# Performance work log

Hardware: AMD Instinct MI355X
Metric: run time of the kernel (lower is better)

Reference implementation:

```python
import jax, jax.numpy as jnp
import numpy as np

N = 8192
D = 512
H = 256
K_TOPK = 21  # k + 1 with k = 20
EPS_NORM = 1e-12
EPS_DEG = 1e-10


def setup_inputs() -> dict:
    key = jax.random.key(0)
    ks = jax.random.split(key, 10)
    s = 0.02  # small init scale so similarities are well-behaved
    return {
        "features": jax.random.normal(ks[0], (N, D), jnp.float32),
        "masked_features": jax.random.normal(ks[1], (N, D), jnp.float32),
        "W1": jax.random.normal(ks[2], (D, D), jnp.float32) * s,
        "b1": jax.random.normal(ks[3], (D,), jnp.float32) * s,
        "W2": jax.random.normal(ks[4], (D, D), jnp.float32) * s,
        "b2": jax.random.normal(ks[5], (D,), jnp.float32) * s,
        "Wg1": jax.random.normal(ks[6], (D, H), jnp.float32) * s,
        "bg1": jax.random.normal(ks[7], (H,), jnp.float32) * s,
        "Wg2": jax.random.normal(ks[8], (H, D), jnp.float32) * s,
        "bg2": jax.random.normal(ks[9], (D,), jnp.float32) * s,
    }


def reference(features, masked_features, W1, b1, W2, b2, Wg1, bg1, Wg2, bg2):
    # ---- graph generator MLP ----
    h = jax.nn.relu(features @ W1 + b1)            # [N, D]
    emb = h @ W2 + b2                              # [N, D]
    norm = jnp.linalg.norm(emb, axis=1, keepdims=True)
    emb = emb / jnp.maximum(norm, EPS_NORM)        # F.normalize(dim=1, p=2)
    sim = emb @ emb.T                              # [N, N] cosine similarity

    # ---- top-k mask (k+1 neighbors), zero diagonal ----
    _, idx = jax.lax.top_k(sim, K_TOPK)            # [N, K]
    rows = jnp.arange(N)[:, None]
    mask = jnp.zeros((N, N), sim.dtype).at[rows, idx].set(1.0)
    mask = mask * (1.0 - jnp.eye(N, dtype=sim.dtype))  # fill_diagonal_(0)
    mask = jax.lax.stop_gradient(mask)
    sim = jax.nn.relu(sim * mask)

    # ---- symmetrize ----
    gen_adj = (sim + sim.T) * 0.5                  # [N, N]

    # ---- degree norm: D^{-1/2} (A + I) D^{-1/2} ----
    A = gen_adj + jnp.eye(N, dtype=gen_adj.dtype)
    inv_sqrt_deg = 1.0 / (jnp.sqrt(A.sum(axis=1)) + EPS_DEG)
    A = inv_sqrt_deg[:, None] * A * inv_sqrt_deg[None, :]

    # ---- two dense GCN hops (dropout inert in eval mode) ----
    h1 = jax.nn.relu(A @ (masked_features @ Wg1 + bg1))  # [N, H]
    h3 = A @ (h1 @ Wg2 + bg2)                            # [N, D]
    return h3, gen_adj
```

## Files before the change

kernel.cpp:

```cpp
#include <hip/hip_runtime.h>
#include <cstdint>
#include <cstddef>

#define NN 8192
#define DD 512
#define HH 256
#define KTOP 21
#define CCAP 192
#define CMIN 48
#define ECAP 224
#define NBIN 1024
#define BFLOOR 1

typedef __attribute__((ext_vector_type(8))) __bf16 bf16x8;
typedef __attribute__((ext_vector_type(4))) float f32x4;

__device__ __forceinline__ unsigned short f2bf(float x) {
    unsigned u = __float_as_uint(x);
    u += 0x7fffu + ((u >> 16) & 1u);
    return (unsigned short)(u >> 16);
}
__device__ __forceinline__ float bf2f(unsigned short h) {
    return __uint_as_float(((unsigned)h) << 16);
}
__device__ __forceinline__ unsigned ordkey(float x) {
    unsigned b = __float_as_uint(x);
    return b ^ (((int)b >> 31) | 0x80000000u);
}

#define GLD16(gp, lp) __builtin_amdgcn_global_load_lds( \
    (const __attribute__((address_space(1))) unsigned int*)(gp), \
    (__attribute__((address_space(3))) unsigned int*)(lp), 16, 0, 0)

template<bool TRANSB, int ACT>
__global__ __launch_bounds__(256)
void sgemm128(const float* __restrict__ A, const float* __restrict__ B,
              const float* __restrict__ bias, float* __restrict__ C,
              int M, int N, int K) {
    constexpr int BM = 128, BN = 128, BK = 16;
    __shared__ float As[BK][BM + 4];
    __shared__ float Bs[BK][BN + 4];

    const int tiles_n = N / BN;
    const int by = blockIdx.x / tiles_n;
    const int bx = blockIdx.x % tiles_n;
    const int row0 = by * BM, col0 = bx * BN;
    const int tid = threadIdx.x;
    const int tx = tid & 15, ty = tid >> 4;

    float acc[8][8];
#pragma unroll
    for (int m = 0; m < 8; ++m)
#pragma unroll
        for (int n = 0; n < 8; ++n) acc[m][n] = 0.f;

    for (int k0 = 0; k0 < K; k0 += BK) {
#pragma unroll
        for (int l = 0; l < 2; ++l) {
            int f = tid + l * 256;
            int r = f >> 2, c4 = f & 3;
            float4 v = *reinterpret_cast<const float4*>(
                A + (size_t)(row0 + r) * K + k0 + c4 * 4);
            As[c4 * 4 + 0][r] = v.x;
            As[c4 * 4 + 1][r] = v.y;
            As[c4 * 4 + 2][r] = v.z;
            As[c4 * 4 + 3][r] = v.w;
        }
        if (TRANSB) {
#pragma unroll
            for (int l = 0; l < 2; ++l) {
                int f = tid + l * 256;
                int r = f >> 2, c4 = f & 3;
                float4 v = *reinterpret_cast<const float4*>(
                    B + (size_t)(col0 + r) * K + k0 + c4 * 4);
                Bs[c4 * 4 + 0][r] = v.x;
                Bs[c4 * 4 + 1][r] = v.y;
                Bs[c4 * 4 + 2][r] = v.z;
                Bs[c4 * 4 + 3][r] = v.w;
            }
        } else {
#pragma unroll
            for (int l = 0; l < 2; ++l) {
                int f = tid + l * 256;
                int kr = f >> 5, n4 = f & 31;
                *reinterpret_cast<float4*>(&Bs[kr][n4 * 4]) =
                    *reinterpret_cast<const float4*>(
                        B + (size_t)(k0 + kr) * N + col0 + n4 * 4);
            }
        }
        __syncthreads();

#pragma unroll
        for (int kk = 0; kk < BK; ++kk) {
            float a[8], b[8];
            *(float4*)&a[0] = *(const float4*)&As[kk][ty * 8];
            *(float4*)&a[4] = *(const float4*)&As[kk][ty * 8 + 4];
            *(float4*)&b[0] = *(const float4*)&Bs[kk][tx * 8];
            *(float4*)&b[4] = *(const float4*)&Bs[kk][tx * 8 + 4];
#pragma unroll
            for (int m = 0; m < 8; ++m)
#pragma unroll
                for (int n = 0; n < 8; ++n)
                    acc[m][n] = fmaf(a[m], b[n], acc[m][n]);
        }
        __syncthreads();
    }

    const int crow = row0 + ty * 8;
    const int ccol = col0 + tx * 8;
    float bv[8];
#pragma unroll
    for (int n = 0; n < 8; ++n) bv[n] = bias ? bias[ccol + n] : 0.f;
#pragma unroll
    for (int m = 0; m < 8; ++m) {
        float o[8];
#pragma unroll
        for (int n = 0; n < 8; ++n) {
            float t = acc[m][n] + bv[n];
            if (ACT == 1) t = fmaxf(t, 0.f);
            o[n] = t;
        }
        *reinterpret_cast<float4*>(C + (size_t)(crow + m) * N + ccol)     = *(float4*)&o[0];
        *reinterpret_cast<float4*>(C + (size_t)(crow + m) * N + ccol + 4) = *(float4*)&o[4];
    }
}

__global__ __launch_bounds__(256)
void rownorm_emit_kernel(float* __restrict__ emb, unsigned short* __restrict__ ehi) {
    const int row = blockIdx.x, tid = threadIdx.x;
    float* rp = emb + (size_t)row * DD;
    float v0 = rp[tid], v1 = rp[tid + 256];
    float sum = v0 * v0 + v1 * v1;
#pragma unroll
    for (int off = 32; off > 0; off >>= 1) sum += __shfl_down(sum, off, 64);
    __shared__ float ws[4];
    __shared__ float sc_sh;
    if ((tid & 63) == 0) ws[tid >> 6] = sum;
    __syncthreads();
    if (tid == 0) {
        float n = sqrtf(ws[0] + ws[1] + ws[2] + ws[3]);
        sc_sh = 1.0f / fmaxf(n, 1e-12f);
    }
    __syncthreads();
    float sc = sc_sh;
    v0 *= sc; v1 *= sc;
    rp[tid] = v0;
    rp[tid + 256] = v1;
    ehi[(size_t)row * DD + tid]       = f2bf(v0);
    ehi[(size_t)row * DD + tid + 256] = f2bf(v1);
}

__global__ __launch_bounds__(256)
void split_kernel(const float* __restrict__ e, unsigned short* __restrict__ hi,
                  unsigned short* __restrict__ lo) {
    const int i = (blockIdx.x * 256 + threadIdx.x) * 4;
    float4 v = *reinterpret_cast<const float4*>(e + i);
    ushort4 h, l;
    h.x = f2bf(v.x); l.x = f2bf(v.x - bf2f(h.x));
    h.y = f2bf(v.y); l.y = f2bf(v.y - bf2f(h.y));
    h.z = f2bf(v.z); l.z = f2bf(v.z - bf2f(h.z));
    h.w = f2bf(v.w); l.w = f2bf(v.w - bf2f(h.w));
    *reinterpret_cast<ushort4*>(hi + i) = h;
    *reinterpret_cast<ushort4*>(lo + i) = l;
}

__global__ __launch_bounds__(256)
void wtrans_kernel(const float* __restrict__ W, unsigned short* __restrict__ Thi,
                   unsigned short* __restrict__ Tlo, int K, int N) {
    int t = blockIdx.x * 256 + threadIdx.x;
    if (t >= K * N) return;
    int k = t / N, n = t - k * N;
    float x = W[t];
    unsigned short h = f2bf(x);
    Thi[(size_t)n * K + k] = h;
    Tlo[(size_t)n * K + k] = f2bf(x - bf2f(h));
}

__global__ __launch_bounds__(256)
void simgemm_bf16(const unsigned short* __restrict__ Ehi,
                  unsigned short* __restrict__ Cb) {
    const int bid = blockIdx.x;
    const int swz = (bid & 7) * 512 + (bid >> 3);
    const int by = swz >> 6, bx = swz & 63;

    __shared__ unsigned short SB[8192];
    unsigned short* Ah = SB;
    unsigned short* Bh = SB + 4096;

    const int tid = threadIdx.x, lane = tid & 63, wid = tid >> 6;
    const int wm = wid >> 1, wn = wid & 1;
    const int fr = lane & 15, fq = lane >> 4;
    const int lrow = lane >> 2;
    const int lcol8 = (lane & 3) * 8;

    const size_t arow0 = (size_t)by * 128;
    const size_t brow0 = (size_t)bx * 128;

    f32x4 acc[4][4];
#pragma unroll
    for (int m = 0; m < 4; ++m)
#pragma unroll
        for (int n = 0; n < 4; ++n) acc[m][n] = (f32x4){0.f, 0.f, 0.f, 0.f};

    for (int k0 = 0; k0 < DD; k0 += 32) {
#pragma unroll
        for (int i = 0; i < 2; ++i) {
            const int chunk = wid + i * 4;
            const int grow = chunk * 16 + lrow;
            GLD16(Ehi + (arow0 + grow) * DD + (k0 + lcol8), Ah + chunk * 512);
            GLD16(Ehi + (brow0 + grow) * DD + (k0 + lcol8), Bh + chunk * 512);
        }
        __syncthreads();

        bf16x8 ah[4], bh[4];
#pragma unroll
        for (int mf = 0; mf < 4; ++mf)
            ah[mf] = *(const bf16x8*)&Ah[(wm * 64 + mf * 16 + fr) * 32 + fq * 8];
#pragma unroll
        for (int nf = 0; nf < 4; ++nf)
            bh[nf] = *(const bf16x8*)&Bh[(wn * 64 + nf * 16 + fr) * 32 + fq * 8];
#pragma unroll
        for (int mf = 0; mf < 4; ++mf)
#pragma unroll
            for (int nf = 0; nf < 4; ++nf)
                acc[mf][nf] = __builtin_amdgcn_mfma_f32_16x16x32_bf16(ah[mf], bh[nf], acc[mf][nf], 0, 0, 0);
        __syncthreads();
    }

#pragma unroll
    for (int ph = 0; ph < 2; ++ph) {
        if (wm == ph) {
#pragma unroll
            for (int mf = 0; mf < 4; ++mf)
#pragma unroll
                for (int nf = 0; nf < 4; ++nf)
#pragma unroll
                    for (int r2 = 0; r2 < 4; ++r2)
                        SB[(mf * 16 + fq * 4 + r2) * 128 + wn * 64 + nf * 16 + fr] =
                            f2bf(acc[mf][nf][r2]);
        }
        __syncthreads();
#pragma unroll
        for (int it = 0; it < 4; ++it) {
            int flat = it * 256 + tid;
            int rowL = flat >> 4, cc = flat & 15;
            *reinterpret_cast<uint4*>(
                &Cb[(arow0 + ph * 64 + rowL) * NN + (size_t)bx * 128 + cc * 8]) =
                *reinterpret_cast<const uint4*>(&SB[rowL * 128 + cc * 8]);
        }
        __syncthreads();
    }
}

template<int KDIM>
__global__ __launch_bounds__(256)
void mfma_nt_bias(const unsigned short* __restrict__ Ahi,
                  const unsigned short* __restrict__ Alo,
                  const unsigned short* __restrict__ Bhi,
                  const unsigned short* __restrict__ Blo,
                  const float* __restrict__ bias, float* __restrict__ C, int N) {
    const int tiles_n = N / 128;
    const int by = blockIdx.x / tiles_n, bx = blockIdx.x % tiles_n;

    __shared__ unsigned short Ah[128 * 32];
    __shared__ unsigned short Al[128 * 32];
    __shared__ unsigned short Bh[128 * 32];
    __shared__ unsigned short Bl[128 * 32];

    const int tid = threadIdx.x, lane = tid & 63, wid = tid >> 6;
    const int wm = wid >> 1, wn = wid & 1;
    const int fr = lane & 15, fq = lane >> 4;
    const int lrow = lane >> 2;
    const int lcol8 = (lane & 3) * 8;

    const size_t arow0 = (size_t)by * 128;
    const size_t brow0 = (size_t)bx * 128;

    f32x4 acc[4][4];
#pragma unroll
    for (int m = 0; m < 4; ++m)
#pragma unroll
        for (int n = 0; n < 4; ++n) acc[m][n] = (f32x4){0.f, 0.f, 0.f, 0.f};

    for (int k0 = 0; k0 < KDIM; k0 += 32) {
#pragma unroll
        for (int i = 0; i < 2; ++i) {
            const int chunk = wid + i * 4;
            const int grow = chunk * 16 + lrow;
            GLD16(Ahi + (arow0 + grow) * KDIM + (k0 + lcol8), Ah + chunk * 512);
            GLD16(Alo + (arow0 + grow) * KDIM + (k0 + lcol8), Al + chunk * 512);
            GLD16(Bhi + (brow0 + grow) * KDIM + (k0 + lcol8), Bh + chunk * 512);
            GLD16(Blo + (brow0 + grow) * KDIM + (k0 + lcol8), Bl + chunk * 512);
        }
        __syncthreads();

        bf16x8 ah[4], al[4], bh[4], bl[4];
#pragma unroll
        for (int mf = 0; mf < 4; ++mf) {
            const int r = wm * 64 + mf * 16 + fr;
            ah[mf] = *(const bf16x8*)&Ah[r * 32 + fq * 8];
            al[mf] = *(const bf16x8*)&Al[r * 32 + fq * 8];
        }
#pragma unroll
        for (int nf = 0; nf < 4; ++nf) {
            const int r = wn * 64 + nf * 16 + fr;
            bh[nf] = *(const bf16x8*)&Bh[r * 32 + fq * 8];
            bl[nf] = *(const bf16x8*)&Bl[r * 32 + fq * 8];
        }
#pragma unroll
        for (int mf = 0; mf < 4; ++mf)
#pragma unroll
            for (int nf = 0; nf < 4; ++nf) {
                acc[mf][nf] = __builtin_amdgcn_mfma_f32_16x16x32_bf16(ah[mf], bh[nf], acc[mf][nf], 0, 0, 0);
                acc[mf][nf] = __builtin_amdgcn_mfma_f32_16x16x32_bf16(ah[mf], bl[nf], acc[mf][nf], 0, 0, 0);
                acc[mf][nf] = __builtin_amdgcn_mfma_f32_16x16x32_bf16(al[mf], bh[nf], acc[mf][nf], 0, 0, 0);
            }
        __syncthreads();
    }

#pragma unroll
    for (int mf = 0; mf < 4; ++mf) {
#pragma unroll
        for (int nf = 0; nf < 4; ++nf) {
            const size_t row = arow0 + wm * 64 + mf * 16 + fq * 4;
            const int col = bx * 128 + wn * 64 + nf * 16 + fr;
            const float bv = bias[col];
#pragma unroll
            for (int r2 = 0; r2 < 4; ++r2)
                C[(row + r2) * N + col] = acc[mf][nf][r2] + bv;
        }
    }
}

__global__ __launch_bounds__(256)
void topk_refine_kernel(const unsigned short* __restrict__ simb,
                        const float* __restrict__ emb,
                        int* __restrict__ tidx, float* __restrict__ tval,
                        int* __restrict__ ecnt, int* __restrict__ elj,
                        float* __restrict__ elv) {
    const int row = blockIdx.x;
    const int tid = threadIdx.x;
    const int lane = tid & 63, wave = tid >> 6;

    const uint4* rp = reinterpret_cast<const uint4*>(simb + (size_t)row * NN);
    uint4 q[4];
#pragma unroll
    for (int t = 0; t < 4; ++t) q[t] = rp[t * 256 + tid];
    unsigned pk[16];
#pragma unroll
    for (int t = 0; t < 4; ++t) {
        pk[t * 4 + 0] = q[t].x; pk[t * 4 + 1] = q[t].y;
        pk[t * 4 + 2] = q[t].z; pk[t * 4 + 3] = q[t].w;
    }

    __shared__ int hist[NBIN];
    for (int b = tid; b < NBIN; b += 256) hist[b] = 0;
    __syncthreads();

    short bins[32];
#pragma unroll
    for (int u = 0; u < 16; ++u) {
        float flo = __uint_as_float(pk[u] << 16);
        float fhi = __uint_as_float(pk[u] & 0xFFFF0000u);
        int blo = (int)(flo * (float)NBIN); blo = max(0, min(NBIN - 1, blo));
        int bhi = (int)(fhi * (float)NBIN); bhi = max(0, min(NBIN - 1, bhi));
        bins[u * 2]     = (short)blo;
        bins[u * 2 + 1] = (short)bhi;
        if (blo >= BFLOOR) atomicAdd(&hist[blo], 1);
        if (bhi >= BFLOOR) atomicAdd(&hist[bhi], 1);
    }
    __syncthreads();

    __shared__ int s_bstar;
    if (wave == 0) {
        int cum = 0, found = -1;
        for (int c0 = NBIN - 1; c0 >= 0 && found < 0; c0 -= 64) {
            int b = c0 - lane;
            int cnt = (b >= 0) ? hist[b] : 0;
            int sc = cnt;
#pragma unroll
            for (int off = 1; off < 64; off <<= 1) {
                int o = __shfl_up(sc, off, 64);
                if (lane >= off) sc += o;
            }
            int chunk_total = __shfl(sc, 63, 64);
            bool hit = (cum + sc >= CMIN);
            unsigned long long mh = __ballot(hit);
            if (mh) found = c0 - (__ffsll((long long)mh) - 1);
            else cum += chunk_total;
        }
        if (found < 0) found = 0;
        if (lane == 0) s_bstar = found;
    }
    __syncthreads();
    const int bstar = s_bstar;

    __shared__ int s_cand[CCAP];
    int cnt = 0;
#pragma unroll
    for (int i = 0; i < 32; ++i) cnt += (bins[i] >= bstar) ? 1 : 0;
    int sc = cnt;
#pragma unroll
    for (int off = 1; off < 64; off <<= 1) {
        int o = __shfl_up(sc, off, 64);
        if (lane >= off) sc += o;
    }
    __shared__ int wtot[4];
    if (lane == 63) wtot[wave] = sc;
    __syncthreads();
    int base = sc - cnt;
#pragma unroll
    for (int w = 0; w < 4; ++w)
        if (w < wave) base += wtot[w];
    int total = wtot[0] + wtot[1] + wtot[2] + wtot[3];

    int pos = base;
#pragma unroll
    for (int u = 0; u < 16; ++u) {
#pragma unroll
        for (int h = 0; h < 2; ++h) {
            if (bins[u * 2 + h] >= bstar) {
                if (pos < CCAP)
                    s_cand[pos] = ((u >> 2) * 256 + tid) * 8 + (u & 3) * 2 + h;
                pos++;
            }
        }
    }
    __syncthreads();
    const int ncand = min(total, CCAP);

    __shared__ float sval[CCAP];
    __shared__ int   sidx[CCAP];
    const float* ei = emb + (size_t)row * DD;
    float4 a0 = reinterpret_cast<const float4*>(ei)[lane * 2];
    float4 a1 = reinterpret_cast<const float4*>(ei)[lane * 2 + 1];

    for (int base2 = wave * 2; base2 < ncand; base2 += 8) {
#pragma unroll
        for (int qq = 0; qq < 2; ++qq) {
            int c = base2 + qq;
            if (c >= ncand) break;
            const int j = s_cand[c];
            const float* ej = emb + (size_t)j * DD;
            float4 b0 = reinterpret_cast<const float4*>(ej)[lane * 2];
            float4 b1 = reinterpret_cast<const float4*>(ej)[lane * 2 + 1];
            float s = 0.f;
            s = fmaf(a0.x, b0.x, s); s = fmaf(a0.y, b0.y, s);
            s = fmaf(a0.z, b0.z, s); s = fmaf(a0.w, b0.w, s);
            s = fmaf(a1.x, b1.x, s); s = fmaf(a1.y, b1.y, s);
            s = fmaf(a1.z, b1.z, s); s = fmaf(a1.w, b1.w, s);
#pragma unroll
            for (int off = 32; off > 0; off >>= 1) s += __shfl_xor(s, off, 64);
            if (lane == 0) { sval[c] = s; sidx[c] = j; }
        }
    }
    __syncthreads();

    __shared__ float selv[KTOP];
    __shared__ int   seli[KTOP];
    if (wave == 0) {
        float v[3]; int id[3];
#pragma unroll
        for (int k = 0; k < 3; ++k) {
            int s = lane + 64 * k;
            if (s < ncand) { v[k] = sval[s]; id[k] = sidx[s]; }
            else           { v[k] = -INFINITY; id[k] = 0x7fffffff; }
        }
#pragma unroll 1
        for (int sel = 0; sel < KTOP; ++sel) {
            float bv = v[0]; int bi = id[0];
#pragma unroll
            for (int k = 1; k < 3; ++k)
                if (v[k] > bv || (v[k] == bv && id[k] < bi)) { bv = v[k]; bi = id[k]; }
#pragma unroll
            for (int off = 1; off < 64; off <<= 1) {
                float ov = __shfl_xor(bv, off, 64);
                int   oi = __shfl_xor(bi, off, 64);
                if (ov > bv || (ov == bv && oi < bi)) { bv = ov; bi = oi; }
            }
            if (lane == 0) { selv[sel] = bv; seli[sel] = bi; }
#pragma unroll
            for (int k = 0; k < 3; ++k)
                if (id[k] == bi) { v[k] = -INFINITY; id[k] = 0x7fffffff; }
        }
    }
    __syncthreads();

    if (tid < KTOP) {
        float bv = selv[tid];
        int   bi = seli[tid];
        tval[(size_t)row * KTOP + tid] = bv;
        tidx[(size_t)row * KTOP + tid] = bi;
        if (bi != row && bi >= 0 && bi < NN && bv > 0.f) {
            float v = bv * 0.5f;
            int pi = atomicAdd(ecnt + row, 1);
            if (pi < ECAP) { elj[(size_t)row * ECAP + pi] = bi; elv[(size_t)row * ECAP + pi] = v; }
            int pj = atomicAdd(ecnt + bi, 1);
            if (pj < ECAP) { elj[(size_t)bi * ECAP + pj] = row; elv[(size_t)bi * ECAP + pj] = v; }
        }
    }
}

__global__ __launch_bounds__(256)
void sort_write_kernel(int* __restrict__ ej, float* __restrict__ ev,
                       const int* __restrict__ ecnt,
                       float* __restrict__ adj, float* __restrict__ sdeg) {
    const int row = blockIdx.x, tid = threadIdx.x;
    const int nraw = ecnt[row];

    float4* out4 = reinterpret_cast<float4*>(adj + (size_t)row * NN);
    const float4 z = {0.f, 0.f, 0.f, 0.f};
#pragma unroll
    for (int f = tid; f < NN / 4; f += 256) out4[f] = z;

    if (nraw > ECAP) return;

    const int n = nraw;
    __shared__ int   lj[ECAP];
    __shared__ float lv[ECAP];
    __shared__ unsigned long long skey[ECAP];
    __shared__ int   oj[ECAP];
    __shared__ float ov[ECAP];
    if (tid < n) {
        int  jv = ej[(size_t)row * ECAP + tid];
        float vv = ev[(size_t)row * ECAP + tid];
        lj[tid] = jv; lv[tid] = vv;
        skey[tid] = ((unsigned long long)(unsigned)jv << 32) | (unsigned long long)ordkey(vv);
    }
    __syncthreads();
    if (tid < n) {
        unsigned long long mk = skey[tid];
        int rank = 0;
        for (int u = 0; u < n; ++u) {
            unsigned long long ku = skey[u];
            rank += (ku < mk || (ku == mk && u < tid)) ? 1 : 0;
        }
        oj[rank] = lj[tid];
        ov[rank] = lv[tid];
    }
    __syncthreads();
    if (tid < n) {
        ej[(size_t)row * ECAP + tid] = oj[tid];
        ev[(size_t)row * ECAP + tid] = ov[tid];
    }
    if (tid == 0) {
        float deg = 1.0f;
        for (int e = 0; e < n; ++e) deg += ov[e];
        sdeg[row] = 1.0f / (sqrtf(deg) + 1e-10f);
    }
    __syncthreads();
    if (tid < n) {
        int j = oj[tid];
        if (tid == 0 || oj[tid - 1] != j) {
            float s = ov[tid];
            if (tid + 1 < n && oj[tid + 1] == j) s += ov[tid + 1];
            adj[(size_t)row * NN + j] = s;
        }
    }
}

__global__ __launch_bounds__(256)
void ovf_fix_kernel(const int* __restrict__ tidx, const float* __restrict__ tval,
                    const int* __restrict__ ecnt, float* __restrict__ adj) {
    int t = blockIdx.x * 256 + threadIdx.x;
    if (t >= NN * KTOP) return;
    int i = t / KTOP;
    int j = tidx[t];
    if (j == i || j < 0) return;
    float v = tval[t];
    if (v <= 0.f) return;
    v *= 0.5f;
    if (ecnt[i] > ECAP) atomicAdd(adj + (size_t)i * NN + j, v);
    if (ecnt[j] > ECAP) atomicAdd(adj + (size_t)j * NN + i, v);
}

__global__ __launch_bounds__(256)
void ovf_deg_kernel(const int* __restrict__ ecnt, const float* __restrict__ adj,
                    float* __restrict__ sdeg) {
    const int row = blockIdx.x, tid = threadIdx.x;
    if (ecnt[row] <= ECAP) return;
    const int lane = tid & 63, wave = tid >> 6;
    const float4* rp = reinterpret_cast<const float4*>(adj + (size_t)row * NN);
    float sum = 0.f;
    for (int f = tid; f < NN / 4; f += 256) {
        float4 v = rp[f];
        sum += (v.x + v.y) + (v.z + v.w);
    }
#pragma unroll
    for (int off = 32; off > 0; off >>= 1) sum += __shfl_down(sum, off, 64);
    __shared__ float ws[4];
    if (lane == 0) ws[wave] = sum;
    __syncthreads();
    if (tid == 0)
        sdeg[row] = 1.0f / (sqrtf(1.0f + ws[0] + ws[1] + ws[2] + ws[3]) + 1e-10f);
}

template<int COLS, bool DORELU>
__global__ __launch_bounds__(256)
void spmm_edges(const int* __restrict__ ej, const float* __restrict__ ev,
                const int* __restrict__ ecnt, const float* __restrict__ adj,
                const float* __restrict__ sdeg,
                const float* __restrict__ X, float* __restrict__ Y) {
    constexpr int CPT = COLS / 256;
    const int i = blockIdx.x;
    const int tid = threadIdx.x;
    const int lane = tid & 63, wave = tid >> 6;
    const float si = sdeg[i];
    const int nraw = ecnt[i];

    float acc[CPT];
#pragma unroll
    for (int c = 0; c < CPT; ++c) acc[c] = 0.f;

    if (nraw <= ECAP) {
        __shared__ int   s_j[ECAP];
        __shared__ float s_w[ECAP];
        if (tid < nraw) {
            int j = ej[(size_t)i * ECAP + tid];
            s_j[tid] = j;
            s_w[tid] = ev[(size_t)i * ECAP + tid] * sdeg[j];
        }
        __syncthreads();
#pragma unroll 4
        for (int e = 0; e < nraw; ++e) {
            int j = s_j[e];
            float we = s_w[e];
#pragma unroll
            for (int c = 0; c < CPT; ++c)
                acc[c] += we * X[(size_t)j * COLS + tid + c * 256];
        }
    } else {
        __shared__ int   s_j[256];
        __shared__ float s_w[256];
        __shared__ int   s_cnt[4];
        const float* rowp = adj + (size_t)i * NN;
        for (int j0 = 0; j0 < NN; j0 += 256) {
            float w = rowp[j0 + tid];
            bool nz = (w != 0.f);
            unsigned long long m = __ballot(nz);
            unsigned long long ltmask = (lane == 0) ? 0ull : (~0ull >> (64 - lane));
            int pre = __popcll(m & ltmask);
            if (lane == 0) s_cnt[wave] = __popcll(m);
            __syncthreads();
            int base = 0;
#pragma unroll
            for (int q = 0; q < 4; ++q)
                if (q < wave) base += s_cnt[q];
            int total = s_cnt[0] + s_cnt[1] + s_cnt[2] + s_cnt[3];
            if (nz) {
                int p = base + pre;
                s_j[p] = j0 + tid;
                s_w[p] = w * sdeg[j0 + tid];
            }
            __syncthreads();
            for (int e = 0; e < total; ++e) {
                int j = s_j[e];
                float we = s_w[e];
#pragma unroll
                for (int c = 0; c < CPT; ++c)
                    acc[c] += we * X[(size_t)j * COLS + tid + c * 256];
            }
            __syncthreads();
        }
    }

#pragma unroll
    for (int c = 0; c < CPT; ++c) {
        float val = si * (acc[c] + si * X[(size_t)i * COLS + tid + c * 256]);
        if (DORELU) val = fmaxf(val, 0.f);
        Y[(size_t)i * COLS + tid + c * 256] = val;
    }
}

extern "C" void kernel_launch(void* const* d_in, const int* in_sizes, int n_in,
                              void* d_out, int out_size, void* d_ws, size_t ws_size,
                              hipStream_t stream) {
    const float* features = (const float*)d_in[0];
    const float* masked   = (const float*)d_in[1];
    const float* W1  = (const float*)d_in[2];
    const float* b1  = (const float*)d_in[3];
    const float* W2  = (const float*)d_in[4];
    const float* b2  = (const float*)d_in[5];
    const float* Wg1 = (const float*)d_in[6];
    const float* bg1 = (const float*)d_in[7];
    const float* Wg2 = (const float*)d_in[8];
    const float* bg2 = (const float*)d_in[9];

    float* out_h3  = (float*)d_out;
    float* out_adj = (float*)d_out + (size_t)NN * DD;
    unsigned short* simb = (unsigned short*)out_adj;

    float* Areg = (float*)d_ws;
    float* Breg = Areg + (size_t)NN * DD;
    float* tail = Breg + (size_t)NN * DD;

    float* h    = Areg;
    unsigned short* ehi = (unsigned short*)Areg;
    unsigned short* mhi = (unsigned short*)Areg;
    unsigned short* mlo = mhi + (size_t)NN * DD;
    unsigned short* h1hi = (unsigned short*)Areg;
    unsigned short* h1lo = h1hi + (size_t)NN * HH;

    float* emb = Breg;
    float* x1  = Breg;
    float* h1  = Breg + (size_t)NN * HH;
    float* x2  = Breg;

    float* tval = tail;
    int*   tidx = (int*)(tval + (size_t)NN * KTOP);
    float* sdeg = (float*)(tidx + (size_t)NN * KTOP);
    int*   ecnt = (int*)(sdeg + NN);
    int*   elj  = ecnt + NN;
    float* elv  = (float*)(elj + (size_t)NN * ECAP);
    unsigned short* wt1hi = (unsigned short*)(elv + (size_t)NN * ECAP);
    unsigned short* wt1lo = wt1hi + (size_t)HH * DD;
    unsigned short* wt2hi = wt1lo + (size_t)HH * DD;
    unsigned short* wt2lo = wt2hi + (size_t)DD * HH;

    dim3 blk(256);

    sgemm128<false, 1><<<dim3((NN / 128) * (DD / 128)), blk, 0, stream>>>(
        features, W1, b1, h, NN, DD, DD);
    sgemm128<false, 0><<<dim3((NN / 128) * (DD / 128)), blk, 0, stream>>>(
        h, W2, b2, emb, NN, DD, DD);
    rownorm_emit_kernel<<<dim3(NN), blk, 0, stream>>>(emb, ehi);
    simgemm_bf16<<<dim3(4096), blk, 0, stream>>>(ehi, simb);
    hipMemsetAsync(ecnt, 0, (size_t)NN * sizeof(int), stream);
    topk_refine_kernel<<<dim3(NN), blk, 0, stream>>>(
        simb, emb, tidx, tval, ecnt, elj, elv);
    sort_write_kernel<<<dim3(NN), blk, 0, stream>>>(elj, elv, ecnt, out_adj, sdeg);
    ovf_fix_kernel<<<dim3((NN * KTOP + 255) / 256), blk, 0, stream>>>(
        tidx, tval, ecnt, out_adj);
    ovf_deg_kernel<<<dim3(NN), blk, 0, stream>>>(ecnt, out_adj, sdeg);
    split_kernel<<<dim3(NN * DD / 1024), blk, 0, stream>>>(masked, mhi, mlo);
    wtrans_kernel<<<dim3(DD * HH / 256), blk, 0, stream>>>(Wg1, wt1hi, wt1lo, DD, HH);
    mfma_nt_bias<DD><<<dim3((NN / 128) * (HH / 128)), blk, 0, stream>>>(
        mhi, mlo, wt1hi, wt1lo, bg1, x1, HH);
    spmm_edges<HH, true><<<dim3(NN), blk, 0, stream>>>(
        elj, elv, ecnt, out_adj, sdeg, x1, h1);
    split_kernel<<<dim3(NN * HH / 1024), blk, 0, stream>>>(h1, h1hi, h1lo);
    wtrans_kernel<<<dim3(HH * DD / 256), blk, 0, stream>>>(Wg2, wt2hi, wt2lo, HH, DD);
    mfma_nt_bias<HH><<<dim3((NN / 128) * (DD / 128)), blk, 0, stream>>>(
        h1hi, h1lo, wt2hi, wt2lo, bg2, x2, DD);
    spmm_edges<DD, false><<<dim3(NN), blk, 0, stream>>>(
        elj, elv, ecnt, out_adj, sdeg, x2, out_h3);
}
```

Baseline: 734.7 us.

## Compute only upper-triangular similarity tiles and mirror them via swizzled LDS transpose

The bf16 similarity GEMM now launches only the 2080 upper-triangular 128x128 tiles. Each off-diagonal tile is written twice, once directly and once transposed through an XOR-swizzled LDS buffer, using the symmetry of emb·embᵀ to cut MFMA work roughly in half. The ecnt memset is folded into the row-norm kernel, and the two weight-transpose kernels are merged into one launch. The cost is a scattered transposed store pattern with 16-byte writes across rows, plus a small serial loop that maps each block index to its tile.

```diff
diff --git a/kernel.cpp b/kernel.cpp
--- a/kernel.cpp
+++ b/kernel.cpp
@@ -11,6 +11,7 @@
 #define ECAP 224
 #define NBIN 1024
 #define BFLOOR 1
+#define NTRI 2080
 
 typedef __attribute__((ext_vector_type(8))) __bf16 bf16x8;
 typedef __attribute__((ext_vector_type(4))) float f32x4;
@@ -27,6 +28,7 @@
     unsigned b = __float_as_uint(x);
     return b ^ (((int)b >> 31) | 0x80000000u);
 }
+__device__ __forceinline__ int swzc(int r, int c) { return c ^ ((r & 7) << 4); }
 
 #define GLD16(gp, lp) __builtin_amdgcn_global_load_lds( \
     (const __attribute__((address_space(1))) unsigned int*)(gp), \
@@ -126,7 +128,8 @@
 }
 
 __global__ __launch_bounds__(256)
-void rownorm_emit_kernel(float* __restrict__ emb, unsigned short* __restrict__ ehi) {
+void rownorm_emit_kernel(float* __restrict__ emb, unsigned short* __restrict__ ehi,
+                         int* __restrict__ ecnt) {
     const int row = blockIdx.x, tid = threadIdx.x;
     float* rp = emb + (size_t)row * DD;
     float v0 = rp[tid], v1 = rp[tid + 256];
@@ -140,6 +143,7 @@
     if (tid == 0) {
         float n = sqrtf(ws[0] + ws[1] + ws[2] + ws[3]);
         sc_sh = 1.0f / fmaxf(n, 1e-12f);
+        ecnt[row] = 0;
     }
     __syncthreads();
     float sc = sc_sh;
@@ -165,23 +169,34 @@
 }
 
 __global__ __launch_bounds__(256)
-void wtrans_kernel(const float* __restrict__ W, unsigned short* __restrict__ Thi,
-                   unsigned short* __restrict__ Tlo, int K, int N) {
+void wtrans2_kernel(const float* __restrict__ Wg1, const float* __restrict__ Wg2,
+                    unsigned short* __restrict__ t1h, unsigned short* __restrict__ t1l,
+                    unsigned short* __restrict__ t2h, unsigned short* __restrict__ t2l) {
     int t = blockIdx.x * 256 + threadIdx.x;
-    if (t >= K * N) return;
-    int k = t / N, n = t - k * N;
-    float x = W[t];
-    unsigned short h = f2bf(x);
-    Thi[(size_t)n * K + k] = h;
-    Tlo[(size_t)n * K + k] = f2bf(x - bf2f(h));
-}
-
-__global__ __launch_bounds__(256)
-void simgemm_bf16(const unsigned short* __restrict__ Ehi,
-                  unsigned short* __restrict__ Cb) {
+    if (t < DD * HH) {
+        int k = t / HH, n = t - k * HH;
+        float x = Wg1[t];
+        unsigned short h = f2bf(x);
+        t1h[(size_t)n * DD + k] = h;
+        t1l[(size_t)n * DD + k] = f2bf(x - bf2f(h));
+    } else {
+        int u = t - DD * HH;
+        int k = u / DD, n = u - k * DD;
+        float x = Wg2[u];
+        unsigned short h = f2bf(x);
+        t2h[(size_t)n * HH + k] = h;
+        t2l[(size_t)n * HH + k] = f2bf(x - bf2f(h));
+    }
+}
+
+__global__ __launch_bounds__(256)
+void simgemm_bf16_tri(const unsigned short* __restrict__ Ehi,
+                      unsigned short* __restrict__ Cb) {
     const int bid = blockIdx.x;
-    const int swz = (bid & 7) * 512 + (bid >> 3);
-    const int by = swz >> 6, bx = swz & 63;
+    const int swz = (bid & 7) * (NTRI / 8) + (bid >> 3);
+    int t = swz, by = 0;
+    while (t >= 64 - by) { t -= 64 - by; ++by; }
+    const int bx = by + t;
 
     __shared__ unsigned short SB[8192];
     unsigned short* Ah = SB;
@@ -235,9 +250,11 @@
 #pragma unroll
                 for (int nf = 0; nf < 4; ++nf)
 #pragma unroll
-                    for (int r2 = 0; r2 < 4; ++r2)
-                        SB[(mf * 16 + fq * 4 + r2) * 128 + wn * 64 + nf * 16 + fr] =
-                            f2bf(acc[mf][nf][r2]);
+                    for (int r2 = 0; r2 < 4; ++r2) {
+                        const int r = mf * 16 + fq * 4 + r2;
+                        const int c = wn * 64 + nf * 16 + fr;
+                        SB[r * 128 + swzc(r, c)] = f2bf(acc[mf][nf][r2]);
+                    }
         }
         __syncthreads();
 #pragma unroll
@@ -246,7 +263,23 @@
             int rowL = flat >> 4, cc = flat & 15;
             *reinterpret_cast<uint4*>(
                 &Cb[(arow0 + ph * 64 + rowL) * NN + (size_t)bx * 128 + cc * 8]) =
-                *reinterpret_cast<const uint4*>(&SB[rowL * 128 + cc * 8]);
+                *reinterpret_cast<const uint4*>(&SB[rowL * 128 + swzc(rowL, cc * 8)]);
+        }
+        if (bx != by) {
+#pragma unroll
+            for (int it = 0; it < 4; ++it) {
+                int w = it * 256 + tid;
+                int c = w & 127, s = w >> 7;
+                unsigned short vals[8];
+#pragma unroll
+                for (int k = 0; k < 8; ++k) {
+                    const int r = s * 8 + k;
+                    vals[k] = SB[r * 128 + swzc(r, c)];
+                }
+                *reinterpret_cast<uint4*>(
+                    &Cb[(brow0 + c) * NN + arow0 + ph * 64 + s * 8]) =
+                    *reinterpret_cast<const uint4*>(&vals[0]);
+            }
         }
         __syncthreads();
     }
@@ -723,9 +756,8 @@
         features, W1, b1, h, NN, DD, DD);
     sgemm128<false, 0><<<dim3((NN / 128) * (DD / 128)), blk, 0, stream>>>(
         h, W2, b2, emb, NN, DD, DD);
-    rownorm_emit_kernel<<<dim3(NN), blk, 0, stream>>>(emb, ehi);
-    simgemm_bf16<<<dim3(4096), blk, 0, stream>>>(ehi, simb);
-    hipMemsetAsync(ecnt, 0, (size_t)NN * sizeof(int), stream);
+    rownorm_emit_kernel<<<dim3(NN), blk, 0, stream>>>(emb, ehi, ecnt);
+    simgemm_bf16_tri<<<dim3(NTRI), blk, 0, stream>>>(ehi, simb);
     topk_refine_kernel<<<dim3(NN), blk, 0, stream>>>(
         simb, emb, tidx, tval, ecnt, elj, elv);
     sort_write_kernel<<<dim3(NN), blk, 0, stream>>>(elj, elv, ecnt, out_adj, sdeg);
@@ -733,13 +765,13 @@
         tidx, tval, ecnt, out_adj);
     ovf_deg_kernel<<<dim3(NN), blk, 0, stream>>>(ecnt, out_adj, sdeg);
     split_kernel<<<dim3(NN * DD / 1024), blk, 0, stream>>>(masked, mhi, mlo);
-    wtrans_kernel<<<dim3(DD * HH / 256), blk, 0, stream>>>(Wg1, wt1hi, wt1lo, DD, HH);
+    wtrans2_kernel<<<dim3(2 * DD * HH / 256), blk, 0, stream>>>(
+        Wg1, Wg2, wt1hi, wt1lo, wt2hi, wt2lo);
     mfma_nt_bias<DD><<<dim3((NN / 128) * (HH / 128)), blk, 0, stream>>>(
         mhi, mlo, wt1hi, wt1lo, bg1, x1, HH);
     spmm_edges<HH, true><<<dim3(NN), blk, 0, stream>>>(
         elj, elv, ecnt, out_adj, sdeg, x1, h1);
     split_kernel<<<dim3(NN * HH / 1024), blk, 0, stream>>>(h1, h1hi, h1lo);
-    wtrans_kernel<<<dim3(HH * DD / 256), blk, 0, stream>>>(Wg2, wt2hi, wt2lo, HH, DD);
     mfma_nt_bias<HH><<<dim3((NN / 128) * (DD / 128)), blk, 0, stream>>>(
         h1hi, h1lo, wt2hi, wt2lo, bg2, x2, DD);
     spmm_edges<DD, false><<<dim3(NN), blk, 0, stream>>>(
```

Result: no change. 732.4 us (-0.3%).
